# Performance work log

Hardware: AMD Instinct MI355X
Metric: run time of the kernel (lower is better)

The kernel has to match this reference:

```python
import jax, jax.numpy as jnp
import numpy as np

EMB = 128
EA = 32
ET = 32
NN = 50000
NE = 320000
NBAND = 3
LAM = 0.01  # softshrink sparsity_threshold
LN_EPS = 1e-5


def _softshrink(x, lam=LAM):
    return jnp.where(x > lam, x - lam, jnp.where(x < -lam, x + lam, jnp.zeros_like(x)))


def _forward(hidden, edge_attr, edge_time_emb, boundary_condition,
             alpha, r1, i1, rb1, ib1, fre_w, fre_b,
             comb_w, comb_b, lin_w, lin_b, ln_g, ln_b, edge_index):
    num_nodes = hidden.shape[0]
    # gather source node features and concat edge features -> [E, d_in]
    x = jnp.concatenate([hidden[edge_index[0]], edge_attr, edge_time_emb], axis=1)
    # FreMLP: FFT over feature dim (real input -> complex64)
    x_fft = jnp.fft.fft(x)
    xr, xi = x_fft.real, x_fft.imag
    energy = jnp.sum(xr * xr + xi * xi, axis=-1)  # [E]
    energy_sum = jnp.sum(energy)
    outs = []
    for k in range(NBAND):
        factor = (2.0 * (k + 1) - 1.0) / (2.0 * NBAND)
        Qk = alpha[k] * factor * energy_sum
        bk = energy_sum / (alpha[k] * (2.0 * NBAND))
        mask = ((energy >= Qk - bk) & (energy <= Qk + bk)).astype(x.dtype)[:, None]
        fr = xr * mask
        fi = xi * mask
        # complex linear: (fr + i*fi) @ (r1 + i*i1) + (rb1 + i*ib1)
        o_r = fr @ r1[k] - fi @ i1[k] + rb1[k]
        o_i = fi @ r1[k] + fr @ i1[k] + ib1[k]
        o_r = _softshrink(jax.nn.relu(o_r))
        o_i = _softshrink(jax.nn.relu(o_i))
        outs.append(jax.lax.complex(o_r, o_i))
    y_fft = jnp.concatenate(outs, axis=-1)  # [E, NBAND*EMB] complex
    y = jnp.fft.ifft(y_fft).real
    msg = y @ fre_w + fre_b  # [E, EMB]
    # view_as_complex(msg, 0) -> view_as_real -> flatten: interleave real with zeros
    msg_ri = jnp.stack([msg, jnp.zeros_like(msg)], axis=-1).reshape(msg.shape[0], 2 * EMB)
    msg2 = msg_ri @ comb_w + comb_b  # [E, EMB]
    # scatter-reduce(sum) into destination nodes + boundary self-loops
    msg_aug = jnp.concatenate([msg2, boundary_condition], axis=0)
    idx_aug = jnp.concatenate([edge_index[1], jnp.arange(num_nodes, dtype=edge_index.dtype)])
    out = jax.ops.segment_sum(msg_aug, idx_aug, num_segments=num_nodes)
    out = out @ lin_w + lin_b
    mu = jnp.mean(out, axis=-1, keepdims=True)
    var = jnp.mean((out - mu) ** 2, axis=-1, keepdims=True)
    out = (out - mu) * jax.lax.rsqrt(var + LN_EPS) * ln_g + ln_b
    return jax.nn.relu(out)  # dropout is identity in eval mode


def setup_inputs() -> dict:
    key = jax.random.key(0)
    ks = jax.random.split(key, 16)
    d_in = EMB + EA + ET
    s = 0.02
    return {
        "hidden": jax.random.normal(ks[0], (NN, EMB), jnp.float32),
        "edge_attr": jax.random.normal(ks[1], (NE, EA), jnp.float32),
        "edge_time_emb": jax.random.normal(ks[2], (NE, ET), jnp.float32),
        "boundary_condition": jax.random.normal(ks[3], (NN, EMB), jnp.float32),
        "alpha": jnp.ones((NBAND,), jnp.float32),
        "r1": s * jax.random.normal(ks[4], (NBAND, d_in, EMB), jnp.float32),
        "i1": s * jax.random.normal(ks[5], (NBAND, d_in, EMB), jnp.float32),
        "rb1": s * jax.random.normal(ks[6], (NBAND, EMB), jnp.float32),
        "ib1": s * jax.random.normal(ks[7], (NBAND, EMB), jnp.float32),
        "fre_w": s * jax.random.normal(ks[8], (NBAND * EMB, EMB), jnp.float32),
        "fre_b": s * jax.random.normal(ks[9], (EMB,), jnp.float32),
        "comb_w": s * jax.random.normal(ks[10], (2 * EMB, EMB), jnp.float32),
        "comb_b": s * jax.random.normal(ks[11], (EMB,), jnp.float32),
        "lin_w": s * jax.random.normal(ks[12], (EMB, EMB), jnp.float32),
        "lin_b": s * jax.random.normal(ks[13], (EMB,), jnp.float32),
        "ln_g": jnp.ones((EMB,), jnp.float32),
        "ln_b": jnp.zeros((EMB,), jnp.float32),
        "edge_index": jax.random.randint(ks[14], (2, NE), 0, NN, dtype=jnp.int32),
    }


def reference(hidden, edge_attr, edge_time_emb, boundary_condition, alpha, r1, i1, rb1, ib1,
              fre_w, fre_b, comb_w, comb_b, lin_w, lin_b, ln_g, ln_b, edge_index):
    return _forward(hidden, edge_attr, edge_time_emb, boundary_condition, alpha, r1, i1,
                    rb1, ib1, fre_w, fre_b, comb_w, comb_b, lin_w, lin_b, ln_g, ln_b, edge_index)
```

## Files before the change

### kernel.cpp

```cpp
#include <hip/hip_runtime.h>
#include <hip/hip_bf16.h>

#define NNODES 50000
#define NEDGES 320000
#define EMB 128
#define DIN 192
#define NB 3
#define LAM 0.01f
#define LN_EPS 1e-5f
#define PI_F 3.14159265358979323846f

#define SCAN_B 196
#define SCAN_N (SCAN_B * 256)

#define TILES (NEDGES / 64)
#define EGRID 250
#define EITER (TILES / EGRID)

typedef __attribute__((ext_vector_type(8))) short v8s;
typedef __attribute__((ext_vector_type(4))) float v4f;
typedef __attribute__((ext_vector_type(2))) float v2f;

#define WS_ESUM 0
#define WS_WB   16
#define WS_G2B  (WS_WB + 73728)
#define WS_G2   (WS_G2B + 49152)
#define WS_PHI  (WS_G2 + 98304)
#define WS_M    (WS_PHI + 98304)
#define WS_BB   (WS_M + 16384)
#define WS_GB2  (WS_BB + 768)
#define WS_CK   (WS_GB2 + 128)
#define WS_EN   (WS_CK + 384)
#define WS_NORM (WS_EN + NEDGES)
#define WS_CNT  (WS_NORM + NNODES)
#define WS_CUR  (WS_CNT + SCAN_N)
#define WS_PART (WS_CUR + SCAN_N)
#define WS_EIDS (WS_PART + 256)

__device__ __forceinline__ unsigned pk2(float a, float b) {
  __hip_bfloat162 h2 = __float22bfloat162_rn(make_float2(a, b));
  return *reinterpret_cast<unsigned*>(&h2);
}

__device__ __forceinline__ void atomic2(float* dp, float a, float b) {
#if __has_builtin(__builtin_amdgcn_flat_atomic_fadd_v2f32)
  v2f val; val.x = a; val.y = b;
  __builtin_amdgcn_flat_atomic_fadd_v2f32((v2f*)dp, val);
#else
  atomicAdd(dp, a); atomicAdd(dp + 1, b);
#endif
}

__device__ __forceinline__ void bar_lds() {
  asm volatile("s_waitcnt lgkmcnt(0)" ::: "memory");
  __builtin_amdgcn_s_barrier();
  asm volatile("" ::: "memory");
}

__global__ __launch_bounds__(256) void k_prep1(
    const float* __restrict__ r1, const float* __restrict__ i1,
    __hip_bfloat16* __restrict__ Wb, const float* __restrict__ comb_w,
    const float* __restrict__ lin_w, float* __restrict__ M,
    const float* __restrict__ fre_w, float* __restrict__ Phi,
    const float* __restrict__ hidden, float* __restrict__ norms,
    float* __restrict__ outz, int* __restrict__ cnt, float* __restrict__ esum) {
  __shared__ float cs[384], sn[384];
  const int t = threadIdx.x;
  const int b = blockIdx.x;
  if (b < 576) {
    if (t < 192) sincosf((2.f * PI_F / 192.f) * (float)t, &sn[t], &cs[t]);
    __syncthreads();
    int idx = b * 256 + t;
    int n = idx / 768, c = idx - (idx / 768) * 768;
    int k = c >> 8, col = c & 255;
    int isI = col >> 7, j = col & 127;
    const float* ap = (isI ? i1 : r1) + (size_t)k * DIN * EMB + j;
    const float* bp = (isI ? r1 : i1) + (size_t)k * DIN * EMB + j;
    float sgn = isI ? -1.f : 1.f;
    float acc = 0.f;
    int m = 0;
    for (int f = 0; f < DIN; ++f) {
      acc = fmaf(cs[m], ap[(size_t)f * EMB], fmaf(sgn * sn[m], bp[(size_t)f * EMB], acc));
      m += n; if (m >= 192) m -= 192;
    }
    int kc = n >> 5, quad = (n & 31) >> 3, jj = n & 7;
    int lane = quad * 16 + (col & 15);
    Wb[((((k * 6 + kc) * 16 + (col >> 4)) * 64) + lane) * 8 + jj] = __float2bfloat16(acc);
  } else if (b < 640) {
    int idx = (b - 576) * 256 + t;
    int j = idx >> 7, j2 = idx & 127;
    float acc = 0.f;
    for (int tt = 0; tt < 128; ++tt)
      acc = fmaf(comb_w[(2 * j) * 128 + tt], lin_w[tt * 128 + j2], acc);
    M[idx] = acc;
  } else if (b < 1024) {
    for (int i = t; i < 384; i += 256)
      sincosf((2.f * PI_F / 384.f) * (float)i, &sn[i], &cs[i]);
    __syncthreads();
    int idx = (b - 640) * 256 + t;
    int slot = idx >> 7, j1 = idx & 127;
    int k = slot >> 8, r = slot & 255;
    int isI = r >> 7;
    int f = k * 128 + (r & 127);
    const float* tp = isI ? sn : cs;
    float sg = isI ? -1.f : 1.f;
    float acc = 0.f;
    int m = 0;
    for (int n = 0; n < 384; ++n) {
      acc = fmaf(sg * tp[m], fre_w[n * 128 + j1], acc);
      m += f; if (m >= 384) m -= 384;
    }
    Phi[slot * 128 + j1] = acc * (1.f / 384.f);
  } else if (b < 13524) {
    const int w = t >> 6, lane = t & 63;
    const int n = (b - 1024) * 4 + w;
    const float2 v = ((const float2*)(hidden + (size_t)n * 128))[lane];
    float ss = v.x * v.x + v.y * v.y;
#pragma unroll
    for (int off = 32; off > 0; off >>= 1) ss += __shfl_xor(ss, off, 64);
    if (lane == 0) norms[n] = ss;
    float2 z; z.x = 0.f; z.y = 0.f;
    ((float2*)(outz + (size_t)n * 128))[lane] = z;
  } else if (b < 13720) {
    cnt[(b - 13524) * 256 + t] = 0;
  } else {
    if (t < 16) esum[t] = 0.f;
  }
}

__global__ __launch_bounds__(256) void k_prep2(
    const float* __restrict__ Phi, const float* __restrict__ M,
    float* __restrict__ G2, __hip_bfloat16* __restrict__ G2b,
    const float* __restrict__ norms, const float* __restrict__ eattr,
    const float* __restrict__ ett, const int* __restrict__ eidx,
    float* __restrict__ energies, float* __restrict__ esum,
    int* __restrict__ cnt) {
  const int t = threadIdx.x;
  const int b = blockIdx.x;
  if (b < 384) {
    int idx = b * 256 + t;
    int slot = idx >> 7, j2 = idx & 127;
    float acc = 0.f;
    for (int j1 = 0; j1 < 128; ++j1)
      acc = fmaf(Phi[slot * 128 + j1], M[j1 * 128 + j2], acc);
    G2[idx] = acc;
    int k = slot >> 8, s = slot & 255;
    int kc = s >> 5, quad = (s & 31) >> 3, jj = s & 7;
    G2b[((((k * 8 + kc) * 8 + (j2 >> 4)) * 64) + quad * 16 + (j2 & 15)) * 8 + jj] =
        __float2bfloat16(acc);
  } else {
    int e = (b - 384) * 256 + t;
    float ss = norms[eidx[e]];
    const float4* a4 = (const float4*)(eattr + (size_t)e * 32);
#pragma unroll
    for (int i = 0; i < 8; ++i) {
      float4 v = a4[i];
      ss += v.x * v.x + v.y * v.y + v.z * v.z + v.w * v.w;
    }
    const float4* t4 = (const float4*)(ett + (size_t)e * 32);
#pragma unroll
    for (int i = 0; i < 8; ++i) {
      float4 v = t4[i];
      ss += v.x * v.x + v.y * v.y + v.z * v.z + v.w * v.w;
    }
    float en = 192.f * ss;
    energies[e] = en;
    float tot = en;
#pragma unroll
    for (int off = 32; off > 0; off >>= 1) tot += __shfl_down(tot, off, 64);
    if ((t & 63) == 0) atomicAdd(esum, tot);
    atomicAdd(&cnt[eidx[NEDGES + e]], 1);
  }
}

__global__ __launch_bounds__(256) void k_prep3(
    const float* __restrict__ rb1, const float* __restrict__ ib1,
    const float* __restrict__ fre_b, const float* __restrict__ comb_b,
    const float* __restrict__ lin_w, const float* __restrict__ M,
    const float* __restrict__ G2, float* __restrict__ bb,
    float* __restrict__ gb2, float* __restrict__ ck,
    int* __restrict__ cnt, int* __restrict__ part) {
  __shared__ int sm[256];
  const int t = threadIdx.x;
  const int b = blockIdx.x;
  if (b < 5) {
    int idx = b * 256 + t;
    if (idx < 768) {
      int k = idx >> 8, r = idx & 255;
      bb[idx] = (r >= 128) ? ib1[k * 128 + (r & 127)] : rb1[k * 128 + r];
    } else if (idx < 896) {
      int j2 = idx - 768;
      float acc = 0.f;
      for (int j = 0; j < 128; ++j) acc += fre_b[j] * M[j * 128 + j2];
      for (int tt = 0; tt < 128; ++tt) acc += comb_b[tt] * lin_w[tt * 128 + j2];
      gb2[j2] = acc;
    } else if (idx < 1280) {
      int q = idx - 896;
      int k = q >> 7, j2 = q & 127;
      float acc = 0.f;
      for (int j = 0; j < 128; ++j) {
        float vr = rb1[k * 128 + j];
        vr = fmaxf(vr, 0.f); vr = (vr > LAM) ? vr - LAM : 0.f;
        float vi = ib1[k * 128 + j];
        vi = fmaxf(vi, 0.f); vi = (vi > LAM) ? vi - LAM : 0.f;
        acc += vr * G2[(k * 256 + j) * 128 + j2] + vi * G2[(k * 256 + 128 + j) * 128 + j2];
      }
      ck[k * 128 + j2] = acc;
    }
  } else {
    int blk = b - 5;
    int i = blk * 256 + t;
    int v = (i < NNODES) ? cnt[i] : 0;
    sm[t] = v;
    __syncthreads();
#pragma unroll
    for (int off = 1; off < 256; off <<= 1) {
      int x = (t >= off) ? sm[t - off] : 0;
      __syncthreads();
      sm[t] += x;
      __syncthreads();
    }
    cnt[i] = sm[t] - v;
    if (t == 255) part[blk] = sm[t];
  }
}

__global__ __launch_bounds__(256) void k_scan(const int* __restrict__ cnt,
                                              const int* __restrict__ part,
                                              int* __restrict__ cur) {
  __shared__ int sm[256];
  const int t = threadIdx.x;
  const int b = blockIdx.x;
  sm[t] = (t < b) ? part[t] : 0;
  __syncthreads();
#pragma unroll
  for (int off = 128; off > 0; off >>= 1) {
    if (t < off) sm[t] += sm[t + off];
    __syncthreads();
  }
  cur[b * 256 + t] = cnt[b * 256 + t] + sm[0];
}

__global__ __launch_bounds__(256) void k_fill(const int* __restrict__ eidx,
                                              int* __restrict__ cur,
                                              int* __restrict__ eids) {
  int e = blockIdx.x * 256 + threadIdx.x;
  int pos = atomicAdd(&cur[eidx[NEDGES + e]], 1);
  eids[pos] = e;
}

#define XS_STR 200
#define OS_STR 264
#define ZS_STR 130

#define LOADM_PUBLISH(B)                                                       \
  do {                                                                         \
    if (t < 3) tileact[B][t] = 0;                                              \
    if (t < 64) {                                                              \
      eid_s[B][t] = eidA;                                                      \
      srcs[B][t] = srcA;                                                       \
      dsts[B][t] = dstA;                                                       \
      _Pragma("unroll") for (int k = 0; k < NB; ++k) {                         \
        bool m_ = (enA >= lo[k]) && (enA <= hi[k]);                            \
        maskf[B][k][t] = m_ ? 1.f : 0.f;                                       \
        if (m_) atomicOr(&tileact[B][k], 1);                                   \
      }                                                                        \
    }                                                                          \
  } while (0)

#define GATHER(B)                                                              \
  do {                                                                         \
    const int eh = t >> 5, ch = (t & 31) * 4;                                  \
    hr0 = *(const float4*)(hidden + (size_t)srcs[B][eh] * 128 + ch);           \
    hr1 = *(const float4*)(hidden + (size_t)srcs[B][eh + 16] * 128 + ch);      \
    hr2 = *(const float4*)(hidden + (size_t)srcs[B][eh + 32] * 128 + ch);      \
    hr3 = *(const float4*)(hidden + (size_t)srcs[B][eh + 48] * 128 + ch);      \
    const int ea = t >> 4, q = t & 15;                                         \
    const float* p0 = (q < 8) ? eattr + (size_t)eid_s[B][ea] * 32 + q * 4      \
                              : ett + (size_t)eid_s[B][ea] * 32 + (q - 8) * 4; \
    ar0 = *(const float4*)p0;                                                  \
    const float* p1 = (q < 8) ? eattr + (size_t)eid_s[B][ea + 32] * 32 + q * 4 \
                              : ett + (size_t)eid_s[B][ea + 32] * 32 + (q - 8) * 4; \
    ar1 = *(const float4*)p1;                                                  \
  } while (0)

#define WRITEX()                                                               \
  do {                                                                         \
    const int eh = t >> 5, ch = (t & 31) * 4;                                  \
    unsigned* p;                                                               \
    p = (unsigned*)&Xs[eh * XS_STR + ch];                                      \
    p[0] = pk2(hr0.x, hr0.y); p[1] = pk2(hr0.z, hr0.w);                        \
    p = (unsigned*)&Xs[(eh + 16) * XS_STR + ch];                               \
    p[0] = pk2(hr1.x, hr1.y); p[1] = pk2(hr1.z, hr1.w);                        \
    p = (unsigned*)&Xs[(eh + 32) * XS_STR + ch];                               \
    p[0] = pk2(hr2.x, hr2.y); p[1] = pk2(hr2.z, hr2.w);                        \
    p = (unsigned*)&Xs[(eh + 48) * XS_STR + ch];                               \
    p[0] = pk2(hr3.x, hr3.y); p[1] = pk2(hr3.z, hr3.w);                        \
    const int ea = t >> 4, q4 = (t & 15) * 4;                                  \
    p = (unsigned*)&Xs[ea * XS_STR + 128 + q4];                                \
    p[0] = pk2(ar0.x, ar0.y); p[1] = pk2(ar0.z, ar0.w);                        \
    p = (unsigned*)&Xs[(ea + 32) * XS_STR + 128 + q4];                         \
    p[0] = pk2(ar1.x, ar1.y); p[1] = pk2(ar1.z, ar1.w);                        \
  } while (0)

__global__ __launch_bounds__(512, 2) void k_edges(
    const float* __restrict__ hidden, const float* __restrict__ eattr,
    const float* __restrict__ ett, const float* __restrict__ alpha,
    const int* __restrict__ eidx, const int* __restrict__ eids,
    const __hip_bfloat16* __restrict__ Wb, const __hip_bfloat16* __restrict__ G2b,
    const float* __restrict__ bb, const float* __restrict__ gb2,
    const float* __restrict__ ck, const float* __restrict__ energies,
    const float* __restrict__ esum, float* __restrict__ accum) {
  __shared__ __align__(16) char smem[64 * XS_STR * 2 + 64 * OS_STR * 2];
  short* Xs = (short*)smem;
  short* Os = (short*)(smem + 64 * XS_STR * 2);
  float* Zs = (float*)smem;
  __shared__ float maskf[2][3][64];
  __shared__ int eid_s[2][64], srcs[2][64], dsts[2][64];
  __shared__ int tileact[2][3];

  const int t = threadIdx.x;
  const int lane = t & 63, w = t >> 6;
  const int quad = lane >> 4, lc = lane & 15;
  const int tile = blockIdx.x;

  float lo[NB], hi[NB];
  {
    const float es = *esum;
#pragma unroll
    for (int k = 0; k < NB; ++k) {
      float a = alpha[k];
      float factor = (2.f * (k + 1) - 1.f) / (2.f * NB);
      float Q = a * factor * es;
      float bw = es / (a * (2.f * NB));
      lo[k] = Q - bw;
      hi[k] = Q + bw;
    }
  }

  float4 hr0, hr1, hr2, hr3, ar0, ar1;
  int eidA = 0, srcA = 0, dstA = 0, eidB = 0;
  float enA = 0.f;

  if (t < 64) {
    int e_ = eids[tile * 64 + t];
    eidA = e_; srcA = eidx[e_]; dstA = eidx[NEDGES + e_]; enA = energies[e_];
  }
  LOADM_PUBLISH(0);
  if (t < 64) {
    int e_ = eids[(tile + EGRID) * 64 + t];
    eidA = e_; srcA = eidx[e_]; dstA = eidx[NEDGES + e_]; enA = energies[e_];
    eidB = eids[(tile + 2 * EGRID) * 64 + t];
  }
  bar_lds();
  GATHER(0);

#pragma unroll 1
  for (int ti = 0; ti < EITER; ++ti) {
    const int cb = ti & 1;
    WRITEX();
    if (ti + 1 < EITER) LOADM_PUBLISH(cb ^ 1);
    if (t < 64) {
      if (ti + 2 < EITER) {
        eidA = eidB;
        srcA = eidx[eidB]; dstA = eidx[NEDGES + eidB]; enA = energies[eidB];
      }
      if (ti + 3 < EITER)
        eidB = eids[(tile + (ti + 3) * EGRID) * 64 + t];
    }
    bar_lds();

    v4f acc2[4];
#pragma unroll
    for (int mt = 0; mt < 4; ++mt)
#pragma unroll
      for (int r = 0; r < 4; ++r) acc2[mt][r] = 0.f;

    for (int k = 0; k < NB; ++k) {
      if (!tileact[cb][k]) continue;
      v4f accA[4][2];
#pragma unroll
      for (int mt = 0; mt < 4; ++mt)
#pragma unroll
        for (int n = 0; n < 2; ++n)
#pragma unroll
          for (int r = 0; r < 4; ++r) accA[mt][n][r] = 0.f;

#pragma unroll
      for (int kc = 0; kc < 6; ++kc) {
        v8s af[4];
#pragma unroll
        for (int mt = 0; mt < 4; ++mt)
          af[mt] = *(const v8s*)&Xs[(mt * 16 + lc) * XS_STR + kc * 32 + quad * 8];
        const __hip_bfloat16* wp = Wb + ((((k * 6 + kc) * 16 + 2 * w) * 64) + lane) * 8;
#pragma unroll
        for (int ntl = 0; ntl < 2; ++ntl) {
          v8s bfr = *(const v8s*)(const void*)(wp + ntl * 512);
#pragma unroll
          for (int mt = 0; mt < 4; ++mt)
            accA[mt][ntl] =
                __builtin_amdgcn_mfma_f32_16x16x32_bf16(af[mt], bfr, accA[mt][ntl], 0, 0, 0);
        }
      }
      bar_lds();
#pragma unroll
      for (int mt = 0; mt < 4; ++mt)
#pragma unroll
        for (int ntl = 0; ntl < 2; ++ntl) {
          int col = w * 32 + ntl * 16 + lc;
          float bbv = bb[k * 256 + col];
#pragma unroll
          for (int reg = 0; reg < 4; ++reg) {
            int row = mt * 16 + quad * 4 + reg;
            float mk = maskf[cb][k][row];
            float v = fmaf(mk, accA[mt][ntl][reg], bbv);
            v = fmaxf(v, 0.f);
            v = (v > LAM) ? v - LAM : 0.f;
            __hip_bfloat16 h = __float2bfloat16(v);
            Os[row * OS_STR + col] = *reinterpret_cast<short*>(&h);
          }
        }
      bar_lds();
#pragma unroll
      for (int kc = 0; kc < 8; ++kc) {
        v8s of[4];
#pragma unroll
        for (int mt = 0; mt < 4; ++mt)
          of[mt] = *(const v8s*)&Os[(mt * 16 + lc) * OS_STR + kc * 32 + quad * 8];
        const __hip_bfloat16* gp = G2b + ((((k * 8 + kc) * 8 + w) * 64) + lane) * 8;
        v8s bfr = *(const v8s*)(const void*)gp;
#pragma unroll
        for (int mt = 0; mt < 4; ++mt)
          acc2[mt] = __builtin_amdgcn_mfma_f32_16x16x32_bf16(of[mt], bfr, acc2[mt], 0, 0, 0);
      }
    }

    if (ti + 1 < EITER) GATHER(cb ^ 1);

    bar_lds();
    {
      int col = w * 16 + lc;
      float base = gb2[col];
#pragma unroll
      for (int k = 0; k < NB; ++k)
        if (!tileact[cb][k]) base += ck[k * 128 + col];
#pragma unroll
      for (int mt = 0; mt < 4; ++mt)
#pragma unroll
        for (int reg = 0; reg < 4; ++reg) {
          int row = mt * 16 + quad * 4 + reg;
          Zs[row * ZS_STR + col] = acc2[mt][reg] + base;
        }
    }
    bar_lds();
    if (w < 4) {
      int c = 2 * lane;
      int r0 = w * 16;
      float s0 = 0.f, s1 = 0.f;
#pragma unroll
      for (int r = 0; r < 16; ++r) {
        int row = r0 + r;
        s0 += Zs[row * ZS_STR + c];
        s1 += Zs[row * ZS_STR + c + 1];
        int d = dsts[cb][row];
        if (r == 15 || dsts[cb][row + 1] != d) {
          atomic2(accum + (size_t)d * 128 + c, s0, s1);
          s0 = 0.f; s1 = 0.f;
        }
      }
    }
    if (ti + 1 < EITER) bar_lds();
  }
}

__global__ __launch_bounds__(256) void k_nodes(const float* __restrict__ boundary,
                                               const float* __restrict__ lin_w,
                                               const float* __restrict__ lin_b,
                                               const float* __restrict__ ln_g,
                                               const float* __restrict__ ln_b,
                                               float* __restrict__ out) {
  __shared__ float lw[32][128];
  const int t = threadIdx.x;
  const int w = t >> 6, lane = t & 63;
  const int n = blockIdx.x * 4 + w;
  float a0 = out[(size_t)n * 128 + lane] + lin_b[lane];
  float a1 = out[(size_t)n * 128 + 64 + lane] + lin_b[64 + lane];
  for (int cb = 0; cb < 128; cb += 32) {
    __syncthreads();
#pragma unroll
    for (int it = 0; it < 16; ++it) {
      int i = t + it * 256;
      lw[i >> 7][i & 127] = lin_w[(cb + (i >> 7)) * 128 + (i & 127)];
    }
    __syncthreads();
#pragma unroll
    for (int r = 0; r < 32; ++r) {
      float bv = boundary[(size_t)n * 128 + cb + r];
      a0 = fmaf(bv, lw[r][lane], a0);
      a1 = fmaf(bv, lw[r][64 + lane], a1);
    }
  }
  float s = a0 + a1, sq = a0 * a0 + a1 * a1;
#pragma unroll
  for (int off = 32; off > 0; off >>= 1) {
    s += __shfl_xor(s, off, 64);
    sq += __shfl_xor(sq, off, 64);
  }
  float mu = s * (1.f / 128.f);
  float var = sq * (1.f / 128.f) - mu * mu;
  float rs = 1.f / sqrtf(var + LN_EPS);
  float y0 = (a0 - mu) * rs * ln_g[lane] + ln_b[lane];
  float y1 = (a1 - mu) * rs * ln_g[64 + lane] + ln_b[64 + lane];
  out[(size_t)n * 128 + lane] = fmaxf(y0, 0.f);
  out[(size_t)n * 128 + 64 + lane] = fmaxf(y1, 0.f);
}

extern "C" void kernel_launch(void* const* d_in, const int* in_sizes, int n_in,
                              void* d_out, int out_size, void* d_ws, size_t ws_size,
                              hipStream_t stream) {
  const float* hidden   = (const float*)d_in[0];
  const float* eattr    = (const float*)d_in[1];
  const float* ett      = (const float*)d_in[2];
  const float* boundary = (const float*)d_in[3];
  const float* alpha    = (const float*)d_in[4];
  const float* r1       = (const float*)d_in[5];
  const float* i1       = (const float*)d_in[6];
  const float* rb1      = (const float*)d_in[7];
  const float* ib1      = (const float*)d_in[8];
  const float* fre_w    = (const float*)d_in[9];
  const float* fre_b    = (const float*)d_in[10];
  const float* comb_w   = (const float*)d_in[11];
  const float* comb_b   = (const float*)d_in[12];
  const float* lin_w    = (const float*)d_in[13];
  const float* lin_b    = (const float*)d_in[14];
  const float* ln_g     = (const float*)d_in[15];
  const float* ln_b     = (const float*)d_in[16];
  const int*   eidx     = (const int*)d_in[17];
  float* ws  = (float*)d_ws;
  float* out = (float*)d_out;
  __hip_bfloat16* Wb  = (__hip_bfloat16*)(ws + WS_WB);
  __hip_bfloat16* G2b = (__hip_bfloat16*)(ws + WS_G2B);
  int* cnt  = (int*)(ws + WS_CNT);
  int* cur  = (int*)(ws + WS_CUR);
  int* part = (int*)(ws + WS_PART);
  int* eids = (int*)(ws + WS_EIDS);

  k_prep1<<<13721, 256, 0, stream>>>(r1, i1, Wb, comb_w, lin_w, ws + WS_M,
                                     fre_w, ws + WS_PHI, hidden, ws + WS_NORM,
                                     out, cnt, ws + WS_ESUM);
  k_prep2<<<384 + NEDGES / 256, 256, 0, stream>>>(ws + WS_PHI, ws + WS_M, ws + WS_G2,
                                                  G2b, ws + WS_NORM, eattr, ett, eidx,
                                                  ws + WS_EN, ws + WS_ESUM, cnt);
  k_prep3<<<5 + SCAN_B, 256, 0, stream>>>(rb1, ib1, fre_b, comb_b, lin_w, ws + WS_M,
                                          ws + WS_G2, ws + WS_BB, ws + WS_GB2,
                                          ws + WS_CK, cnt, part);
  k_scan<<<SCAN_B, 256, 0, stream>>>(cnt, part, cur);
  k_fill<<<NEDGES / 256, 256, 0, stream>>>(eidx, cur, eids);
  k_edges<<<EGRID, 512, 0, stream>>>(hidden, eattr, ett, alpha, eidx, eids,
                                     Wb, G2b, ws + WS_BB, ws + WS_GB2,
                                     ws + WS_CK, ws + WS_EN, ws + WS_ESUM, out);
  k_nodes<<<NNODES / 4, 256, 0, stream>>>(boundary, lin_w, lin_b, ln_g, ln_b, out);
}
```

Before: 525.6 us.

## Use MFMA for node linear, retile edge GEMM2, vectorize LDS stores, double edge grid

The per-node boundary @ lin_w product moves from scalar FMAs to bf16 MFMA tiles of 64 nodes, using lin_w pre-packed into MFMA layout in prep. The second edge GEMM is re-tiled so each wave computes 32 rows by 32 columns with swapped MFMA operands, which lets the epilogues write vectorized float4 and packed bf16 stores to LDS. The edge grid is doubled to 500 blocks and the Zs stride is padded to 132. In exchange, node-side precision drops because boundary and lin_w are rounded to bf16.

After: 483.9 us. -7.9%, faster.

```diff
diff --git a/kernel.cpp b/kernel.cpp
--- a/kernel.cpp
+++ b/kernel.cpp
@@ -14,12 +14,13 @@
 #define SCAN_N (SCAN_B * 256)
 
 #define TILES (NEDGES / 64)
-#define EGRID 250
+#define EGRID 500
 #define EITER (TILES / EGRID)
 
 typedef __attribute__((ext_vector_type(8))) short v8s;
 typedef __attribute__((ext_vector_type(4))) float v4f;
 typedef __attribute__((ext_vector_type(2))) float v2f;
+typedef __attribute__((ext_vector_type(2))) unsigned v2u;
 
 #define WS_ESUM 0
 #define WS_WB   16
@@ -36,6 +37,7 @@
 #define WS_CUR  (WS_CNT + SCAN_N)
 #define WS_PART (WS_CUR + SCAN_N)
 #define WS_EIDS (WS_PART + 256)
+#define WS_LWB  (WS_EIDS + NEDGES)
 
 __device__ __forceinline__ unsigned pk2(float a, float b) {
   __hip_bfloat162 h2 = __float22bfloat162_rn(make_float2(a, b));
@@ -63,7 +65,8 @@
     const float* __restrict__ lin_w, float* __restrict__ M,
     const float* __restrict__ fre_w, float* __restrict__ Phi,
     const float* __restrict__ hidden, float* __restrict__ norms,
-    float* __restrict__ outz, int* __restrict__ cnt, float* __restrict__ esum) {
+    float* __restrict__ outz, int* __restrict__ cnt, float* __restrict__ esum,
+    __hip_bfloat16* __restrict__ lwb) {
   __shared__ float cs[384], sn[384];
   const int t = threadIdx.x;
   const int b = blockIdx.x;
@@ -93,11 +96,17 @@
     for (int tt = 0; tt < 128; ++tt)
       acc = fmaf(comb_w[(2 * j) * 128 + tt], lin_w[tt * 128 + j2], acc);
     M[idx] = acc;
-  } else if (b < 1024) {
+  } else if (b < 704) {
+    int idx = (b - 640) * 256 + t;
+    int kk = idx >> 7, col = idx & 127;
+    int kc = kk >> 5, quad2 = (kk & 31) >> 3, jj = kk & 7;
+    lwb[(((kc * 8 + (col >> 4)) * 64) + quad2 * 16 + (col & 15)) * 8 + jj] =
+        __float2bfloat16(lin_w[kk * 128 + col]);
+  } else if (b < 1088) {
     for (int i = t; i < 384; i += 256)
       sincosf((2.f * PI_F / 384.f) * (float)i, &sn[i], &cs[i]);
     __syncthreads();
-    int idx = (b - 640) * 256 + t;
+    int idx = (b - 704) * 256 + t;
     int slot = idx >> 7, j1 = idx & 127;
     int k = slot >> 8, r = slot & 255;
     int isI = r >> 7;
@@ -111,9 +120,9 @@
       m += f; if (m >= 384) m -= 384;
     }
     Phi[slot * 128 + j1] = acc * (1.f / 384.f);
-  } else if (b < 13524) {
+  } else if (b < 13588) {
     const int w = t >> 6, lane = t & 63;
-    const int n = (b - 1024) * 4 + w;
+    const int n = (b - 1088) * 4 + w;
     const float2 v = ((const float2*)(hidden + (size_t)n * 128))[lane];
     float ss = v.x * v.x + v.y * v.y;
 #pragma unroll
@@ -121,8 +130,8 @@
     if (lane == 0) norms[n] = ss;
     float2 z; z.x = 0.f; z.y = 0.f;
     ((float2*)(outz + (size_t)n * 128))[lane] = z;
-  } else if (b < 13720) {
-    cnt[(b - 13524) * 256 + t] = 0;
+  } else if (b < 13784) {
+    cnt[(b - 13588) * 256 + t] = 0;
   } else {
     if (t < 16) esum[t] = 0.f;
   }
@@ -251,7 +260,7 @@
 
 #define XS_STR 200
 #define OS_STR 264
-#define ZS_STR 130
+#define ZS_STR 132
 
 #define LOADM_PUBLISH(B)                                                       \
   do {                                                                         \
@@ -287,20 +296,20 @@
 #define WRITEX()                                                               \
   do {                                                                         \
     const int eh = t >> 5, ch = (t & 31) * 4;                                  \
-    unsigned* p;                                                               \
-    p = (unsigned*)&Xs[eh * XS_STR + ch];                                      \
-    p[0] = pk2(hr0.x, hr0.y); p[1] = pk2(hr0.z, hr0.w);                        \
-    p = (unsigned*)&Xs[(eh + 16) * XS_STR + ch];                               \
-    p[0] = pk2(hr1.x, hr1.y); p[1] = pk2(hr1.z, hr1.w);                        \
-    p = (unsigned*)&Xs[(eh + 32) * XS_STR + ch];                               \
-    p[0] = pk2(hr2.x, hr2.y); p[1] = pk2(hr2.z, hr2.w);                        \
-    p = (unsigned*)&Xs[(eh + 48) * XS_STR + ch];                               \
-    p[0] = pk2(hr3.x, hr3.y); p[1] = pk2(hr3.z, hr3.w);                        \
+    v2u u;                                                                     \
+    u.x = pk2(hr0.x, hr0.y); u.y = pk2(hr0.z, hr0.w);                          \
+    *(v2u*)&Xs[eh * XS_STR + ch] = u;                                          \
+    u.x = pk2(hr1.x, hr1.y); u.y = pk2(hr1.z, hr1.w);                          \
+    *(v2u*)&Xs[(eh + 16) * XS_STR + ch] = u;                                   \
+    u.x = pk2(hr2.x, hr2.y); u.y = pk2(hr2.z, hr2.w);                          \
+    *(v2u*)&Xs[(eh + 32) * XS_STR + ch] = u;                                   \
+    u.x = pk2(hr3.x, hr3.y); u.y = pk2(hr3.z, hr3.w);                          \
+    *(v2u*)&Xs[(eh + 48) * XS_STR + ch] = u;                                   \
     const int ea = t >> 4, q4 = (t & 15) * 4;                                  \
-    p = (unsigned*)&Xs[ea * XS_STR + 128 + q4];                                \
-    p[0] = pk2(ar0.x, ar0.y); p[1] = pk2(ar0.z, ar0.w);                        \
-    p = (unsigned*)&Xs[(ea + 32) * XS_STR + 128 + q4];                         \
-    p[0] = pk2(ar1.x, ar1.y); p[1] = pk2(ar1.z, ar1.w);                        \
+    u.x = pk2(ar0.x, ar0.y); u.y = pk2(ar0.z, ar0.w);                          \
+    *(v2u*)&Xs[ea * XS_STR + 128 + q4] = u;                                    \
+    u.x = pk2(ar1.x, ar1.y); u.y = pk2(ar1.z, ar1.w);                          \
+    *(v2u*)&Xs[(ea + 32) * XS_STR + 128 + q4] = u;                             \
   } while (0)
 
 __global__ __launch_bounds__(512, 2) void k_edges(
@@ -322,6 +331,7 @@
   const int t = threadIdx.x;
   const int lane = t & 63, w = t >> 6;
   const int quad = lane >> 4, lc = lane & 15;
+  const int we = w >> 2, wc = w & 3;
   const int tile = blockIdx.x;
 
   float lo[NB], hi[NB];
@@ -370,11 +380,13 @@
     }
     bar_lds();
 
-    v4f acc2[4];
-#pragma unroll
-    for (int mt = 0; mt < 4; ++mt)
-#pragma unroll
-      for (int r = 0; r < 4; ++r) acc2[mt][r] = 0.f;
+    v4f acc2[2][2];
+#pragma unroll
+    for (int m2 = 0; m2 < 2; ++m2)
+#pragma unroll
+      for (int ct = 0; ct < 2; ++ct)
+#pragma unroll
+        for (int r = 0; r < 4; ++r) acc2[m2][ct][r] = 0.f;
 
     for (int k = 0; k < NB; ++k) {
       if (!tileact[cb][k]) continue;
@@ -399,58 +411,67 @@
 #pragma unroll
           for (int mt = 0; mt < 4; ++mt)
             accA[mt][ntl] =
-                __builtin_amdgcn_mfma_f32_16x16x32_bf16(af[mt], bfr, accA[mt][ntl], 0, 0, 0);
+                __builtin_amdgcn_mfma_f32_16x16x32_bf16(bfr, af[mt], accA[mt][ntl], 0, 0, 0);
         }
       }
       bar_lds();
 #pragma unroll
-      for (int mt = 0; mt < 4; ++mt)
+      for (int mt = 0; mt < 4; ++mt) {
+        const float mk = maskf[cb][k][mt * 16 + lc];
 #pragma unroll
         for (int ntl = 0; ntl < 2; ++ntl) {
-          int col = w * 32 + ntl * 16 + lc;
-          float bbv = bb[k * 256 + col];
-#pragma unroll
-          for (int reg = 0; reg < 4; ++reg) {
-            int row = mt * 16 + quad * 4 + reg;
-            float mk = maskf[cb][k][row];
-            float v = fmaf(mk, accA[mt][ntl][reg], bbv);
-            v = fmaxf(v, 0.f);
-            v = (v > LAM) ? v - LAM : 0.f;
-            __hip_bfloat16 h = __float2bfloat16(v);
-            Os[row * OS_STR + col] = *reinterpret_cast<short*>(&h);
-          }
+          const int colb = w * 32 + ntl * 16 + quad * 4;
+          const float4 bbv = *(const float4*)&bb[k * 256 + colb];
+          float v0 = fmaf(mk, accA[mt][ntl][0], bbv.x);
+          float v1 = fmaf(mk, accA[mt][ntl][1], bbv.y);
+          float v2 = fmaf(mk, accA[mt][ntl][2], bbv.z);
+          float v3 = fmaf(mk, accA[mt][ntl][3], bbv.w);
+          v0 = fmaxf(v0, 0.f); v0 = (v0 > LAM) ? v0 - LAM : 0.f;
+          v1 = fmaxf(v1, 0.f); v1 = (v1 > LAM) ? v1 - LAM : 0.f;
+          v2 = fmaxf(v2, 0.f); v2 = (v2 > LAM) ? v2 - LAM : 0.f;
+          v3 = fmaxf(v3, 0.f); v3 = (v3 > LAM) ? v3 - LAM : 0.f;
+          v2u u; u.x = pk2(v0, v1); u.y = pk2(v2, v3);
+          *(v2u*)&Os[(mt * 16 + lc) * OS_STR + colb] = u;
         }
+      }
       bar_lds();
 #pragma unroll
       for (int kc = 0; kc < 8; ++kc) {
-        v8s of[4];
-#pragma unroll
-        for (int mt = 0; mt < 4; ++mt)
-          of[mt] = *(const v8s*)&Os[(mt * 16 + lc) * OS_STR + kc * 32 + quad * 8];
-        const __hip_bfloat16* gp = G2b + ((((k * 8 + kc) * 8 + w) * 64) + lane) * 8;
-        v8s bfr = *(const v8s*)(const void*)gp;
-#pragma unroll
-        for (int mt = 0; mt < 4; ++mt)
-          acc2[mt] = __builtin_amdgcn_mfma_f32_16x16x32_bf16(of[mt], bfr, acc2[mt], 0, 0, 0);
+        v8s of0 = *(const v8s*)&Os[(we * 32 + lc) * OS_STR + kc * 32 + quad * 8];
+        v8s of1 = *(const v8s*)&Os[(we * 32 + 16 + lc) * OS_STR + kc * 32 + quad * 8];
+#pragma unroll
+        for (int ct = 0; ct < 2; ++ct) {
+          v8s g = *(const v8s*)(const void*)(
+              G2b + ((((k * 8 + kc) * 8 + (wc * 2 + ct)) * 64) + lane) * 8);
+          acc2[0][ct] = __builtin_amdgcn_mfma_f32_16x16x32_bf16(g, of0, acc2[0][ct], 0, 0, 0);
+          acc2[1][ct] = __builtin_amdgcn_mfma_f32_16x16x32_bf16(g, of1, acc2[1][ct], 0, 0, 0);
+        }
       }
     }
 
     if (ti + 1 < EITER) GATHER(cb ^ 1);
 
     bar_lds();
-    {
-      int col = w * 16 + lc;
-      float base = gb2[col];
+#pragma unroll
+    for (int ct = 0; ct < 2; ++ct) {
+      const int colb = wc * 32 + ct * 16 + quad * 4;
+      float4 base = *(const float4*)&gb2[colb];
 #pragma unroll
       for (int k = 0; k < NB; ++k)
-        if (!tileact[cb][k]) base += ck[k * 128 + col];
-#pragma unroll
-      for (int mt = 0; mt < 4; ++mt)
-#pragma unroll
-        for (int reg = 0; reg < 4; ++reg) {
-          int row = mt * 16 + quad * 4 + reg;
-          Zs[row * ZS_STR + col] = acc2[mt][reg] + base;
+        if (!tileact[cb][k]) {
+          const float4 cv = *(const float4*)&ck[k * 128 + colb];
+          base.x += cv.x; base.y += cv.y; base.z += cv.z; base.w += cv.w;
         }
+#pragma unroll
+      for (int m2 = 0; m2 < 2; ++m2) {
+        const int rowz = we * 32 + m2 * 16 + lc;
+        float4 zz;
+        zz.x = acc2[m2][ct][0] + base.x;
+        zz.y = acc2[m2][ct][1] + base.y;
+        zz.z = acc2[m2][ct][2] + base.z;
+        zz.w = acc2[m2][ct][3] + base.w;
+        *(float4*)&Zs[rowz * ZS_STR + colb] = zz;
+      }
     }
     bar_lds();
     if (w < 4) {
@@ -460,8 +481,8 @@
 #pragma unroll
       for (int r = 0; r < 16; ++r) {
         int row = r0 + r;
-        s0 += Zs[row * ZS_STR + c];
-        s1 += Zs[row * ZS_STR + c + 1];
+        const float2 z = *(const float2*)&Zs[row * ZS_STR + c];
+        s0 += z.x; s1 += z.y;
         int d = dsts[cb][row];
         if (r == 15 || dsts[cb][row + 1] != d) {
           atomic2(accum + (size_t)d * 128 + c, s0, s1);
@@ -473,46 +494,86 @@
   }
 }
 
-__global__ __launch_bounds__(256) void k_nodes(const float* __restrict__ boundary,
-                                               const float* __restrict__ lin_w,
-                                               const float* __restrict__ lin_b,
-                                               const float* __restrict__ ln_g,
-                                               const float* __restrict__ ln_b,
-                                               float* __restrict__ out) {
-  __shared__ float lw[32][128];
+__global__ __launch_bounds__(256) void k_nodes(
+    const float* __restrict__ boundary, const __hip_bfloat16* __restrict__ lwb,
+    const float* __restrict__ lin_b, const float* __restrict__ ln_g,
+    const float* __restrict__ ln_b, float* __restrict__ out) {
+  __shared__ __align__(16) short Bs[64 * 136];
+  __shared__ __align__(16) float Zs[64 * 132];
   const int t = threadIdx.x;
   const int w = t >> 6, lane = t & 63;
-  const int n = blockIdx.x * 4 + w;
-  float a0 = out[(size_t)n * 128 + lane] + lin_b[lane];
-  float a1 = out[(size_t)n * 128 + 64 + lane] + lin_b[64 + lane];
-  for (int cb = 0; cb < 128; cb += 32) {
-    __syncthreads();
-#pragma unroll
-    for (int it = 0; it < 16; ++it) {
-      int i = t + it * 256;
-      lw[i >> 7][i & 127] = lin_w[(cb + (i >> 7)) * 128 + (i & 127)];
-    }
-    __syncthreads();
-#pragma unroll
-    for (int r = 0; r < 32; ++r) {
-      float bv = boundary[(size_t)n * 128 + cb + r];
-      a0 = fmaf(bv, lw[r][lane], a0);
-      a1 = fmaf(bv, lw[r][64 + lane], a1);
-    }
-  }
-  float s = a0 + a1, sq = a0 * a0 + a1 * a1;
-#pragma unroll
-  for (int off = 32; off > 0; off >>= 1) {
-    s += __shfl_xor(s, off, 64);
-    sq += __shfl_xor(sq, off, 64);
-  }
-  float mu = s * (1.f / 128.f);
-  float var = sq * (1.f / 128.f) - mu * mu;
-  float rs = 1.f / sqrtf(var + LN_EPS);
-  float y0 = (a0 - mu) * rs * ln_g[lane] + ln_b[lane];
-  float y1 = (a1 - mu) * rs * ln_g[64 + lane] + ln_b[64 + lane];
-  out[(size_t)n * 128 + lane] = fmaxf(y0, 0.f);
-  out[(size_t)n * 128 + 64 + lane] = fmaxf(y1, 0.f);
+  const int quad = lane >> 4, lc = lane & 15;
+  const int n0 = blockIdx.x * 64;
+#pragma unroll
+  for (int it = 0; it < 8; ++it) {
+    int fi = it * 256 + t;
+    int row = fi >> 5, c4 = fi & 31;
+    float4 v = make_float4(0.f, 0.f, 0.f, 0.f);
+    if (n0 + row < NNODES)
+      v = *(const float4*)(boundary + (size_t)(n0 + row) * 128 + c4 * 4);
+    v2u u; u.x = pk2(v.x, v.y); u.y = pk2(v.z, v.w);
+    *(v2u*)&Bs[row * 136 + c4 * 4] = u;
+  }
+  __syncthreads();
+  const int we = w >> 1, wc = w & 1;
+  v4f acc[2][4];
+#pragma unroll
+  for (int m2 = 0; m2 < 2; ++m2)
+#pragma unroll
+    for (int ct = 0; ct < 4; ++ct)
+#pragma unroll
+      for (int r = 0; r < 4; ++r) acc[m2][ct][r] = 0.f;
+#pragma unroll
+  for (int kc = 0; kc < 4; ++kc) {
+    v8s b0 = *(const v8s*)&Bs[(we * 32 + lc) * 136 + kc * 32 + quad * 8];
+    v8s b1 = *(const v8s*)&Bs[(we * 32 + 16 + lc) * 136 + kc * 32 + quad * 8];
+#pragma unroll
+    for (int ct = 0; ct < 4; ++ct) {
+      v8s af = *(const v8s*)(const void*)(
+          lwb + (((kc * 8 + (wc * 4 + ct)) * 64) + lane) * 8);
+      acc[0][ct] = __builtin_amdgcn_mfma_f32_16x16x32_bf16(af, b0, acc[0][ct], 0, 0, 0);
+      acc[1][ct] = __builtin_amdgcn_mfma_f32_16x16x32_bf16(af, b1, acc[1][ct], 0, 0, 0);
+    }
+  }
+#pragma unroll
+  for (int m2 = 0; m2 < 2; ++m2)
+#pragma unroll
+    for (int ct = 0; ct < 4; ++ct) {
+      const int colb = wc * 64 + ct * 16 + quad * 4;
+      const int row = we * 32 + m2 * 16 + lc;
+      float4 z;
+      z.x = acc[m2][ct][0]; z.y = acc[m2][ct][1];
+      z.z = acc[m2][ct][2]; z.w = acc[m2][ct][3];
+      *(float4*)&Zs[row * 132 + colb] = z;
+    }
+  __syncthreads();
+  const int c = 2 * lane;
+  const float2 lb = *(const float2*)&lin_b[c];
+  const float2 gg = *(const float2*)&ln_g[c];
+  const float2 bbv = *(const float2*)&ln_b[c];
+#pragma unroll 1
+  for (int i = 0; i < 16; ++i) {
+    int row = w * 16 + i;
+    int n = n0 + row;
+    if (n >= NNODES) break;
+    const float2 z = *(const float2*)&Zs[row * 132 + c];
+    const float2 ob = *(const float2*)&out[(size_t)n * 128 + c];
+    float a0 = z.x + ob.x + lb.x;
+    float a1 = z.y + ob.y + lb.y;
+    float s = a0 + a1, sq = a0 * a0 + a1 * a1;
+#pragma unroll
+    for (int off = 32; off > 0; off >>= 1) {
+      s += __shfl_xor(s, off, 64);
+      sq += __shfl_xor(sq, off, 64);
+    }
+    float mu = s * (1.f / 128.f);
+    float var = sq * (1.f / 128.f) - mu * mu;
+    float rs = 1.f / sqrtf(var + LN_EPS);
+    float2 o;
+    o.x = fmaxf((a0 - mu) * rs * gg.x + bbv.x, 0.f);
+    o.y = fmaxf((a1 - mu) * rs * gg.y + bbv.y, 0.f);
+    *(float2*)&out[(size_t)n * 128 + c] = o;
+  }
 }
 
 extern "C" void kernel_launch(void* const* d_in, const int* in_sizes, int n_in,
@@ -540,14 +601,15 @@
   float* out = (float*)d_out;
   __hip_bfloat16* Wb  = (__hip_bfloat16*)(ws + WS_WB);
   __hip_bfloat16* G2b = (__hip_bfloat16*)(ws + WS_G2B);
+  __hip_bfloat16* lwb = (__hip_bfloat16*)(ws + WS_LWB);
   int* cnt  = (int*)(ws + WS_CNT);
   int* cur  = (int*)(ws + WS_CUR);
   int* part = (int*)(ws + WS_PART);
   int* eids = (int*)(ws + WS_EIDS);
 
-  k_prep1<<<13721, 256, 0, stream>>>(r1, i1, Wb, comb_w, lin_w, ws + WS_M,
+  k_prep1<<<13785, 256, 0, stream>>>(r1, i1, Wb, comb_w, lin_w, ws + WS_M,
                                      fre_w, ws + WS_PHI, hidden, ws + WS_NORM,
-                                     out, cnt, ws + WS_ESUM);
+                                     out, cnt, ws + WS_ESUM, lwb);
   k_prep2<<<384 + NEDGES / 256, 256, 0, stream>>>(ws + WS_PHI, ws + WS_M, ws + WS_G2,
                                                   G2b, ws + WS_NORM, eattr, ett, eidx,
                                                   ws + WS_EN, ws + WS_ESUM, cnt);
@@ -559,5 +621,5 @@
   k_edges<<<EGRID, 512, 0, stream>>>(hidden, eattr, ett, alpha, eidx, eids,
                                      Wb, G2b, ws + WS_BB, ws + WS_GB2,
                                      ws + WS_CK, ws + WS_EN, ws + WS_ESUM, out);
-  k_nodes<<<NNODES / 4, 256, 0, stream>>>(boundary, lin_w, lin_b, ln_g, ln_b, out);
-}
+  k_nodes<<<(NNODES + 63) / 64, 256, 0, stream>>>(boundary, lwb, lin_b, ln_g, ln_b, out);
+}
```
